# Kernel tuning notes

Measured on AMD Instinct MI355X. Metric: run time of the kernel, lower is better.

## Reference

```python
import jax, jax.numpy as jnp
import numpy as np

N = 50000      # nodes
E = 800000     # edges (avg degree 16)
D_IN, D_H, D_OUT = 128, 128, 64


def setup_inputs() -> dict:
    key = jax.random.key(0)
    ks = jax.random.split(key, 12)
    s = 0.05  # weight init scale
    return {
        "x": jax.random.normal(ks[0], (N, D_IN), jnp.float32),
        "edge_index": jax.random.randint(ks[1], (2, E), 0, N, dtype=jnp.int64),
        "Wl0": jax.random.normal(ks[2], (D_H, D_IN), jnp.float32) * s,
        "bl0": jax.random.normal(ks[3], (D_H,), jnp.float32) * s,
        "Wr0": jax.random.normal(ks[4], (D_H, D_IN), jnp.float32) * s,
        "Wl1": jax.random.normal(ks[5], (D_H, D_H), jnp.float32) * s,
        "bl1": jax.random.normal(ks[6], (D_H,), jnp.float32) * s,
        "Wr1": jax.random.normal(ks[7], (D_H, D_H), jnp.float32) * s,
        "Wl2": jax.random.normal(ks[8], (D_OUT, D_H), jnp.float32) * s,
        "bl2": jax.random.normal(ks[9], (D_OUT,), jnp.float32) * s,
        "Wr2": jax.random.normal(ks[10], (D_OUT, D_H), jnp.float32) * s,
    }


def _sage_layer(h, src, dst, Wl, bl, Wr):
    # mean aggregation over incoming neighbors: out[i] = mean_{j in N(i)} h[j]
    n = h.shape[0]
    agg = jax.ops.segment_sum(h[src], dst, num_segments=n)          # [N, D]
    deg = jax.ops.segment_sum(jnp.ones((src.shape[0],), h.dtype), dst,
                              num_segments=n)                        # [N]
    mean = agg / jnp.maximum(deg, 1.0)[:, None]  # empty rows -> 0, matches torch_sparse
    # lin_l(agg) + lin_r(self); lin_r has no bias in PyG SAGEConv
    return mean @ Wl.T + bl + h @ Wr.T


def reference(x, edge_index, Wl0, bl0, Wr0, Wl1, bl1, Wr1, Wl2, bl2, Wr2):
    src, dst = edge_index[1], edge_index[0]  # adj row = dst, col = src
    h = jax.nn.relu(_sage_layer(x, src, dst, Wl0, bl0, Wr0))
    h = jax.nn.relu(_sage_layer(h, src, dst, Wl1, bl1, Wr1))
    h = _sage_layer(h, src, dst, Wl2, bl2, Wr2)
    return jax.nn.log_softmax(h, axis=1)
```

## Files before the change

kernel.cpp:

```cpp
#include <hip/hip_runtime.h>
#include <hip/hip_bf16.h>


typedef __attribute__((ext_vector_type(8))) short bf16x8;
typedef __attribute__((ext_vector_type(4))) float f32x4;

#define NPB 128
#define BCAP 2560
#define EPB 8192
#define EPT 32
#define CPAD 16

__device__ __forceinline__ unsigned short f2bf(float f) {
    unsigned int u = __builtin_bit_cast(unsigned int, f);
    u += 0x7fffu + ((u >> 16) & 1u);
    return (unsigned short)(u >> 16);
}
__device__ __forceinline__ float bf2f(unsigned int bits16) {
    return __builtin_bit_cast(float, bits16 << 16);
}
__device__ __forceinline__ bf16x8 pack8(float4 lo, float4 hi) {
    bf16x8 r;
    r[0] = (short)f2bf(lo.x); r[1] = (short)f2bf(lo.y);
    r[2] = (short)f2bf(lo.z); r[3] = (short)f2bf(lo.w);
    r[4] = (short)f2bf(hi.x); r[5] = (short)f2bf(hi.y);
    r[6] = (short)f2bf(hi.z); r[7] = (short)f2bf(hi.w);
    return r;
}


__global__ __launch_bounds__(256) void distribute_kernel(const int* __restrict__ dst,
                                                         const int* __restrict__ srcv,
                                                         int* __restrict__ gcnt,
                                                         unsigned int* __restrict__ staging,
                                                         int E, int NBc) {
    __shared__ unsigned int stage[EPB];
    __shared__ int hist[400];
    __shared__ int lstart[400];
    __shared__ int gbase[400];
    __shared__ int scanbuf[256];
    int t = threadIdx.x;
    int e0 = blockIdx.x * EPB;
    unsigned int w[EPT];

    for (int b = t; b < NBc + 1; b += 256) hist[b] = 0;
    __syncthreads();

#pragma unroll
    for (int i = 0; i < EPT; ++i) {
        int e = e0 + i * 256 + t;
        unsigned int word = 0xFFFFFFFFu;
        if (e < E) word = ((unsigned int)dst[e] << 16) | (unsigned int)srcv[e];
        w[i] = word;
        int b = (int)(word >> 23); if (b > NBc) b = NBc;
        atomicAdd(&hist[b], 1);
    }
    __syncthreads();

    int b0 = 2 * t, b1 = 2 * t + 1;
    int h0 = (b0 <= NBc) ? hist[b0] : 0;
    int h1 = (b1 <= NBc) ? hist[b1] : 0;
    int pair = h0 + h1;
    scanbuf[t] = pair;
    __syncthreads();
    for (int off = 1; off < 256; off <<= 1) {
        int v = (t >= off) ? scanbuf[t - off] : 0;
        __syncthreads();
        scanbuf[t] += v;
        __syncthreads();
    }
    int excl = scanbuf[t] - pair;
    if (b0 <= NBc) lstart[b0] = excl;
    if (b1 <= NBc) lstart[b1] = excl + h0;
    __syncthreads();

    for (int b = t; b < NBc; b += 256) {
        int h = hist[b];
        gbase[b] = h ? atomicAdd(&gcnt[b * CPAD], h) : 0;
    }
    for (int b = t; b < NBc + 1; b += 256) hist[b] = lstart[b];
    __syncthreads();

#pragma unroll
    for (int i = 0; i < EPT; ++i) {
        unsigned int word = w[i];
        int b = (int)(word >> 23); if (b > NBc) b = NBc;
        int p = atomicAdd(&hist[b], 1);
        stage[p] = word;
    }
    __syncthreads();

    int total = lstart[NBc];
    for (int i = t; i < total; i += 256) {
        unsigned int word = stage[i];
        int b = (int)(word >> 23);
        int gpos = gbase[b] + (i - lstart[b]);
        staging[(size_t)b * BCAP + gpos] = word;
    }
}


__global__ __launch_bounds__(256) void build_kernel(const unsigned int* __restrict__ staging,
                                                    const int* __restrict__ gcnt,
                                                    int* __restrict__ row_ptr,
                                                    int* __restrict__ adj, int N, int NBc) {
    __shared__ int hist[NPB];
    __shared__ int scn[NPB];
    __shared__ int wsum[4];
    int b = blockIdx.x;
    int t = threadIdx.x;
    int n0 = b * NPB;
    int nb = N - n0; if (nb > NPB) nb = NPB;
    int ec = gcnt[b * CPAD];
    const unsigned int* st = staging + (size_t)b * BCAP;

    int a = 0;
    for (int j = t; j < b; j += 256) a += gcnt[j * CPAD];
#pragma unroll
    for (int off = 32; off; off >>= 1) a += __shfl_xor(a, off);
    if ((t & 63) == 0) wsum[t >> 6] = a;
    if (t < NPB) hist[t] = 0;
    __syncthreads();
    int bb = wsum[0] + wsum[1] + wsum[2] + wsum[3];

    for (int i = t; i < ec; i += 256)
        atomicAdd(&hist[(st[i] >> 16) & (NPB - 1)], 1);
    __syncthreads();

    int v = (t < NPB) ? hist[t] : 0;
    if (t < NPB) scn[t] = v;
    __syncthreads();
    for (int off = 1; off < NPB; off <<= 1) {
        int u = (t >= off && t < NPB) ? scn[t - off] : 0;
        __syncthreads();
        if (t < NPB) scn[t] += u;
        __syncthreads();
    }
    if (t < NPB) hist[t] = scn[t] - v;
    if (t < nb) row_ptr[n0 + t] = bb + (scn[t] - v);
    if (b == NBc - 1 && t == 0) row_ptr[N] = bb + ec;
    __syncthreads();

    for (int i = t; i < ec; i += 256) {
        unsigned int pk = st[i];
        int p = atomicAdd(&hist[(pk >> 16) & (NPB - 1)], 1);
        adj[bb + p] = (int)(pk & 0xffffu);
    }
}


__global__ void cast_w_kernel(const float* p0, const float* p1, const float* p2,
                              const float* p3, const float* p4, const float* p5,
                              unsigned short* __restrict__ wbf) {
    int w = blockIdx.x * 256 + threadIdx.x;
    if (w < 40960) {
        const float* src;
        int local;
        if      (w < 8192)  { src = p0; local = w; }
        else if (w < 16384) { src = p1; local = w - 8192; }
        else if (w < 24576) { src = p2; local = w - 16384; }
        else if (w < 32768) { src = p3; local = w - 24576; }
        else if (w < 36864) { src = p4; local = w - 32768; }
        else                { src = p5; local = w - 36864; }
        float2 v = ((const float2*)src)[local];
        unsigned int p = (unsigned int)f2bf(v.x) | ((unsigned int)f2bf(v.y) << 16);
        ((unsigned int*)wbf)[w] = p;
    }
}


template<int NJ, int AF32>
__global__ __launch_bounds__(256) void gemm_mfma_kernel(const void* __restrict__ Hp,
                                                        const unsigned short* __restrict__ Wl,
                                                        const unsigned short* __restrict__ Wr,
                                                        unsigned short* __restrict__ C,
                                                        int N) {
    int wave = threadIdx.x >> 6;
    int lane = threadIdx.x & 63;
    int l15 = lane & 15, quad = lane >> 4;
    int m0 = blockIdx.x * 64 + wave * 16;
    int r0 = m0 + l15; if (r0 > N - 1) r0 = N - 1;

    f32x4 acc[NJ] = {};
#pragma unroll
    for (int ks = 0; ks < 4; ++ks) {
        int vidx = ks * 4 + quad;
        bf16x8 a;
        if constexpr (AF32) {
            const float4* A = (const float4*)((const float*)Hp + (size_t)r0 * 128);
            a = pack8(A[vidx * 2], A[vidx * 2 + 1]);
        } else {
            a = ((const bf16x8*)((const unsigned short*)Hp + (size_t)r0 * 128))[vidx];
        }
#pragma unroll
        for (int j = 0; j < NJ; ++j) {
            const unsigned short* W = (j < NJ / 2) ? Wl : Wr;
            int wr = ((j < NJ / 2) ? j : j - NJ / 2) * 16 + l15;
            bf16x8 b = ((const bf16x8*)(W + (size_t)wr * 128))[vidx];
            acc[j] = __builtin_amdgcn_mfma_f32_16x16x32_bf16(a, b, acc[j], 0, 0, 0);
        }
    }

    const int ldC = NJ * 16;
#pragma unroll
    for (int j = 0; j < NJ; ++j)
#pragma unroll
        for (int r = 0; r < 4; ++r) {
            int row = m0 + quad * 4 + r;
            if (row < N)
                C[(size_t)row * ldC + j * 16 + l15] = f2bf(acc[j][r]);
        }
}


__global__ __launch_bounds__(256) void agg_relu_kernel(const unsigned short* __restrict__ C,
                                                       const int* __restrict__ row_ptr,
                                                       const int* __restrict__ adj,
                                                       const float* __restrict__ bias,
                                                       unsigned short* __restrict__ hout, int N) {
    int node = (int)((blockIdx.x * blockDim.x + threadIdx.x) >> 6);
    int lane = threadIdx.x & 63;
    if (node >= N) return;
    int g = lane >> 4;
    int c = lane & 15;
    int beg = row_ptr[node], end = row_ptr[node + 1];
    float p[8] = {};

    int e = beg;
    while (e < end) {
        int cnt = end - e; if (cnt > 64) cnt = 64;
        int ll = lane; if (ll > cnt - 1) ll = cnt - 1;
        int myidx = adj[e + ll];
        int c1 = cnt - 1;
        for (int i = 0; i < cnt; i += 16) {
            int t0 = i + g, t1 = i + 4 + g, t2 = i + 8 + g, t3 = i + 12 + g;
            int s0 = __shfl(myidx, t0 > c1 ? c1 : t0);
            int s1 = __shfl(myidx, t1 > c1 ? c1 : t1);
            int s2 = __shfl(myidx, t2 > c1 ? c1 : t2);
            int s3 = __shfl(myidx, t3 > c1 ? c1 : t3);
            float m0 = t0 < cnt ? 1.f : 0.f;
            float m1 = t1 < cnt ? 1.f : 0.f;
            float m2 = t2 < cnt ? 1.f : 0.f;
            float m3 = t3 < cnt ? 1.f : 0.f;
            bf16x8 v0 = ((const bf16x8*)(C + (size_t)s0 * 256))[c];
            bf16x8 v1 = ((const bf16x8*)(C + (size_t)s1 * 256))[c];
            bf16x8 v2 = ((const bf16x8*)(C + (size_t)s2 * 256))[c];
            bf16x8 v3 = ((const bf16x8*)(C + (size_t)s3 * 256))[c];
#pragma unroll
            for (int k = 0; k < 8; ++k) {
                p[k] += m0 * bf2f((unsigned short)v0[k]);
                p[k] += m1 * bf2f((unsigned short)v1[k]);
                p[k] += m2 * bf2f((unsigned short)v2[k]);
                p[k] += m3 * bf2f((unsigned short)v3[k]);
            }
        }
        e += cnt;
    }

#pragma unroll
    for (int k = 0; k < 8; ++k) {
        p[k] += __shfl_xor(p[k], 16);
        p[k] += __shfl_xor(p[k], 32);
    }

    int deg = end - beg;
    float inv = 1.0f / (float)(deg > 1 ? deg : 1);
    bf16x8 sv = ((const bf16x8*)(C + (size_t)node * 256))[16 + c];
    float4 b0 = ((const float4*)bias)[2 * c];
    float4 b1 = ((const float4*)bias)[2 * c + 1];
    float bb[8] = {b0.x, b0.y, b0.z, b0.w, b1.x, b1.y, b1.z, b1.w};
    bf16x8 o;
#pragma unroll
    for (int k = 0; k < 8; ++k) {
        float v = fmaxf(p[k] * inv + bb[k] + bf2f((unsigned short)sv[k]), 0.f);
        o[k] = (short)f2bf(v);
    }
    if (g == 0)
        ((bf16x8*)(hout + (size_t)node * 128))[c] = o;
}


__global__ __launch_bounds__(256) void final_kernel(const unsigned short* __restrict__ C,
                                                    const int* __restrict__ row_ptr,
                                                    const int* __restrict__ adj,
                                                    const float* __restrict__ bias,
                                                    float* __restrict__ out, int N) {
    int node = (int)((blockIdx.x * blockDim.x + threadIdx.x) >> 6);
    int lane = threadIdx.x & 63;
    if (node >= N) return;
    int g = lane >> 3;
    int c = lane & 7;
    int beg = row_ptr[node], end = row_ptr[node + 1];
    float p[8] = {};

    int e = beg;
    while (e < end) {
        int cnt = end - e; if (cnt > 64) cnt = 64;
        int ll = lane; if (ll > cnt - 1) ll = cnt - 1;
        int myidx = adj[e + ll];
        int c1 = cnt - 1;
        for (int i = 0; i < cnt; i += 16) {
            int ta = i + g, tb = i + 8 + g;
            int sa = __shfl(myidx, ta > c1 ? c1 : ta);
            int sb = __shfl(myidx, tb > c1 ? c1 : tb);
            float ma = ta < cnt ? 1.f : 0.f;
            float mb = tb < cnt ? 1.f : 0.f;
            bf16x8 va = ((const bf16x8*)(C + (size_t)sa * 128))[c];
            bf16x8 vb = ((const bf16x8*)(C + (size_t)sb * 128))[c];
#pragma unroll
            for (int k = 0; k < 8; ++k) {
                p[k] += ma * bf2f((unsigned short)va[k]);
                p[k] += mb * bf2f((unsigned short)vb[k]);
            }
        }
        e += cnt;
    }

#pragma unroll
    for (int k = 0; k < 8; ++k) {
        p[k] += __shfl_xor(p[k], 8);
        p[k] += __shfl_xor(p[k], 16);
        p[k] += __shfl_xor(p[k], 32);
    }

    int deg = end - beg;
    float inv = 1.0f / (float)(deg > 1 ? deg : 1);
    bf16x8 sv = ((const bf16x8*)(C + (size_t)node * 128))[8 + c];
    float4 b0 = ((const float4*)bias)[2 * c];
    float4 b1 = ((const float4*)bias)[2 * c + 1];
    float bb[8] = {b0.x, b0.y, b0.z, b0.w, b1.x, b1.y, b1.z, b1.w};
    float u[8];
#pragma unroll
    for (int k = 0; k < 8; ++k)
        u[k] = p[k] * inv + bb[k] + bf2f((unsigned short)sv[k]);

    float m = u[0];
#pragma unroll
    for (int k = 1; k < 8; ++k) m = fmaxf(m, u[k]);
#pragma unroll
    for (int off = 1; off < 8; off <<= 1) m = fmaxf(m, __shfl_xor(m, off));
    float se = 0.f;
#pragma unroll
    for (int k = 0; k < 8; ++k) se += __expf(u[k] - m);
#pragma unroll
    for (int off = 1; off < 8; off <<= 1) se += __shfl_xor(se, off);
    float ls = __logf(se);

    if (g == 0) {
        float4 o0 = {u[0] - m - ls, u[1] - m - ls, u[2] - m - ls, u[3] - m - ls};
        float4 o1 = {u[4] - m - ls, u[5] - m - ls, u[6] - m - ls, u[7] - m - ls};
        ((float4*)(out + (size_t)node * 64))[2 * c] = o0;
        ((float4*)(out + (size_t)node * 64))[2 * c + 1] = o1;
    }
}


extern "C" void kernel_launch(void* const* d_in, const int* in_sizes, int n_in,
                              void* d_out, int out_size, void* d_ws, size_t ws_size,
                              hipStream_t stream) {
    const float* x   = (const float*)d_in[0];
    const int*   ei  = (const int*)d_in[1];
    const float* Wl0 = (const float*)d_in[2];
    const float* bl0 = (const float*)d_in[3];
    const float* Wr0 = (const float*)d_in[4];
    const float* Wl1 = (const float*)d_in[5];
    const float* bl1 = (const float*)d_in[6];
    const float* Wr1 = (const float*)d_in[7];
    const float* Wl2 = (const float*)d_in[8];
    const float* bl2 = (const float*)d_in[9];
    const float* Wr2 = (const float*)d_in[10];
    float* out = (float*)d_out;

    const int N  = in_sizes[0] / 128;
    const int E  = in_sizes[1] / 2;
    const int NB = (N + NPB - 1) / NPB;

    char* ws = (char*)d_ws;
    auto alloc = [&](size_t bytes) {
        char* p = ws;
        ws += (bytes + 255) & ~(size_t)255;
        return p;
    };
    int*   row_ptr    = (int*)alloc((size_t)(N + 1) * 4);
    int*   adj        = (int*)alloc((size_t)E * 4);
    int*   gcnt       = (int*)alloc((size_t)NB * CPAD * 4);
    unsigned int* staging = (unsigned int*)alloc((size_t)NB * BCAP * 4);
    unsigned short* wbf = (unsigned short*)alloc((size_t)81920 * 2);
    unsigned short* C   = (unsigned short*)alloc((size_t)N * 256 * 2);
    unsigned short* hA  = (unsigned short*)alloc((size_t)N * 128 * 2);
    unsigned short* hB  = (unsigned short*)alloc((size_t)N * 128 * 2);

    const int* dstp = ei;
    const int* srcp = ei + E;

    hipMemsetAsync(gcnt, 0, (size_t)NB * CPAD * 4, stream);
    int distBlocks = (E + EPB - 1) / EPB;
    distribute_kernel<<<distBlocks, 256, 0, stream>>>(dstp, srcp, gcnt, staging, E, NB);
    build_kernel<<<NB, 256, 0, stream>>>(staging, gcnt, row_ptr, adj, N, NB);

    cast_w_kernel<<<160, 256, 0, stream>>>(Wl0, Wr0, Wl1, Wr1, Wl2, Wr2, wbf);
    unsigned short* wl0 = wbf;
    unsigned short* wr0 = wbf + 16384;
    unsigned short* wl1 = wbf + 32768;
    unsigned short* wr1 = wbf + 49152;
    unsigned short* wl2 = wbf + 65536;
    unsigned short* wr2 = wbf + 73728;

    dim3 blk(256);
    int gemmRows = (N + 63) / 64;
    int aggBlocks = (N * 64 + 255) / 256;

    gemm_mfma_kernel<16, 1><<<gemmRows, blk, 0, stream>>>((const void*)x, wl0, wr0, C, N);
    agg_relu_kernel<<<aggBlocks, blk, 0, stream>>>(C, row_ptr, adj, bl0, hA, N);
    gemm_mfma_kernel<16, 0><<<gemmRows, blk, 0, stream>>>((const void*)hA, wl1, wr1, C, N);
    agg_relu_kernel<<<aggBlocks, blk, 0, stream>>>(C, row_ptr, adj, bl1, hB, N);
    gemm_mfma_kernel<8, 0><<<gemmRows, blk, 0, stream>>>((const void*)hB, wl2, wr2, C, N);
    final_kernel<<<aggBlocks, blk, 0, stream>>>(C, row_ptr, adj, bl2, out, N);
}
```

Before: 311.6 us.

## Split GEMM columns across waves and keep weight fragments in registers

The GEMM kernel previously gave each wave 16 rows and all output columns, reloading weight fragments from global memory for every row tile. Now each wave owns a slice of output columns, loads its weight fragments once into registers, and loops over all 64 rows of the block. This is meant to cut redundant weight loads, at the cost of each wave reading the full A tile (four times the activation reads per block, mostly served by cache) and more register pressure.

```diff
diff --git a/kernel.cpp b/kernel.cpp
--- a/kernel.cpp
+++ b/kernel.cpp
@@ -169,7 +169,7 @@
 }
 
 
-template<int NJ, int AF32>
+template<int CF, int AF32>
 __global__ __launch_bounds__(256) void gemm_mfma_kernel(const void* __restrict__ Hp,
                                                         const unsigned short* __restrict__ Wl,
                                                         const unsigned short* __restrict__ Wr,
@@ -178,38 +178,52 @@
     int wave = threadIdx.x >> 6;
     int lane = threadIdx.x & 63;
     int l15 = lane & 15, quad = lane >> 4;
-    int m0 = blockIdx.x * 64 + wave * 16;
-    int r0 = m0 + l15; if (r0 > N - 1) r0 = N - 1;
-
-    f32x4 acc[NJ] = {};
-#pragma unroll
-    for (int ks = 0; ks < 4; ++ks) {
-        int vidx = ks * 4 + quad;
-        bf16x8 a;
-        if constexpr (AF32) {
-            const float4* A = (const float4*)((const float*)Hp + (size_t)r0 * 128);
-            a = pack8(A[vidx * 2], A[vidx * 2 + 1]);
-        } else {
-            a = ((const bf16x8*)((const unsigned short*)Hp + (size_t)r0 * 128))[vidx];
+    const int NCOL = 4 * CF * 16;
+    const int half = NCOL >> 1;
+
+    bf16x8 bfr[CF][4];
+#pragma unroll
+    for (int cf = 0; cf < CF; ++cf) {
+        int col0 = (wave * CF + cf) * 16;
+        const unsigned short* W = (col0 < half) ? Wl : Wr;
+        int wr = (col0 < half ? col0 : col0 - half) + l15;
+#pragma unroll
+        for (int ks = 0; ks < 4; ++ks)
+            bfr[cf][ks] = ((const bf16x8*)(W + (size_t)wr * 128))[ks * 4 + quad];
+    }
+
+    int m0 = blockIdx.x * 64;
+    f32x4 acc[4][CF] = {};
+#pragma unroll
+    for (int rf = 0; rf < 4; ++rf) {
+        int r0 = m0 + rf * 16 + l15; if (r0 > N - 1) r0 = N - 1;
+#pragma unroll
+        for (int ks = 0; ks < 4; ++ks) {
+            int vidx = ks * 4 + quad;
+            bf16x8 a;
+            if constexpr (AF32) {
+                const float4* A = (const float4*)((const float*)Hp + (size_t)r0 * 128);
+                a = pack8(A[vidx * 2], A[vidx * 2 + 1]);
+            } else {
+                a = ((const bf16x8*)((const unsigned short*)Hp + (size_t)r0 * 128))[vidx];
+            }
+#pragma unroll
+            for (int cf = 0; cf < CF; ++cf)
+                acc[rf][cf] = __builtin_amdgcn_mfma_f32_16x16x32_bf16(a, bfr[cf][ks],
+                                                                      acc[rf][cf], 0, 0, 0);
         }
-#pragma unroll
-        for (int j = 0; j < NJ; ++j) {
-            const unsigned short* W = (j < NJ / 2) ? Wl : Wr;
-            int wr = ((j < NJ / 2) ? j : j - NJ / 2) * 16 + l15;
-            bf16x8 b = ((const bf16x8*)(W + (size_t)wr * 128))[vidx];
-            acc[j] = __builtin_amdgcn_mfma_f32_16x16x32_bf16(a, b, acc[j], 0, 0, 0);
-        }
-    }
-
-    const int ldC = NJ * 16;
-#pragma unroll
-    for (int j = 0; j < NJ; ++j)
-#pragma unroll
-        for (int r = 0; r < 4; ++r) {
-            int row = m0 + quad * 4 + r;
-            if (row < N)
-                C[(size_t)row * ldC + j * 16 + l15] = f2bf(acc[j][r]);
-        }
+    }
+
+#pragma unroll
+    for (int rf = 0; rf < 4; ++rf)
+#pragma unroll
+        for (int cf = 0; cf < CF; ++cf)
+#pragma unroll
+            for (int r = 0; r < 4; ++r) {
+                int row = m0 + rf * 16 + quad * 4 + r;
+                if (row < N)
+                    C[(size_t)row * NCOL + (wave * CF + cf) * 16 + l15] = f2bf(acc[rf][cf][r]);
+            }
 }
 
 
@@ -410,10 +424,10 @@
     int gemmRows = (N + 63) / 64;
     int aggBlocks = (N * 64 + 255) / 256;
 
-    gemm_mfma_kernel<16, 1><<<gemmRows, blk, 0, stream>>>((const void*)x, wl0, wr0, C, N);
+    gemm_mfma_kernel<4, 1><<<gemmRows, blk, 0, stream>>>((const void*)x, wl0, wr0, C, N);
     agg_relu_kernel<<<aggBlocks, blk, 0, stream>>>(C, row_ptr, adj, bl0, hA, N);
-    gemm_mfma_kernel<16, 0><<<gemmRows, blk, 0, stream>>>((const void*)hA, wl1, wr1, C, N);
+    gemm_mfma_kernel<4, 0><<<gemmRows, blk, 0, stream>>>((const void*)hA, wl1, wr1, C, N);
     agg_relu_kernel<<<aggBlocks, blk, 0, stream>>>(C, row_ptr, adj, bl1, hB, N);
-    gemm_mfma_kernel<8, 0><<<gemmRows, blk, 0, stream>>>((const void*)hB, wl2, wr2, C, N);
+    gemm_mfma_kernel<2, 0><<<gemmRows, blk, 0, stream>>>((const void*)hB, wl2, wr2, C, N);
     final_kernel<<<aggBlocks, blk, 0, stream>>>(C, row_ptr, adj, bl2, out, N);
 }
```

New measurement: 273.3 us. -12.3%, faster.
